# Kernel optimization log

Measured on AMD Instinct MI355X. Metric: run time of the kernel, lower is better.

Reference implementation:

```python
import jax, jax.numpy as jnp
import numpy as np

TOP_K = 2


def setup_inputs() -> dict:
    key = jax.random.key(0)
    k_x, k_g, k_w1, k_w2, k_w3 = jax.random.split(key, 5)
    B, S, D, H, E = 2, 512, 1024, 512, 8
    x = jax.random.normal(k_x, (B, S, D), dtype=jnp.float32)
    gate_w = jax.random.normal(k_g, (D, E), dtype=jnp.float32) * (D ** -0.5)
    w1 = jax.random.normal(k_w1, (E, D, H), dtype=jnp.float32) * 0.02  # gate proj
    w2 = jax.random.normal(k_w2, (E, H, D), dtype=jnp.float32) * 0.02  # down proj
    w3 = jax.random.normal(k_w3, (E, D, H), dtype=jnp.float32) * 0.02  # up proj
    return {"x": x, "gate_w": gate_w, "w1": w1, "w2": w2, "w3": w3}


def reference(x, gate_w, w1, w2, w3):
    # Token-choice top-k MoE with grouped SwiGLU experts, no shared expert.
    # Equivalent to torchtune MoE: gather routed tokens, scale by top-k router
    # score, run per-expert FFN, scatter-add back. Since each expert's FFN has
    # no bias (FFN(0) == 0), the dispatch/grouped-GEMM/combine is expressed
    # densely as sum_e FFN_e(scale[:, e] * x), which is mathematically identical.
    B, S, D = x.shape
    E = gate_w.shape[1]
    xf = x.reshape(B * S, D)                      # [T, D]
    T = B * S

    logits = xf @ gate_w                          # [T, E]
    scores = jax.nn.softmax(logits, axis=-1)
    top_scores, top_idx = jax.lax.top_k(scores, TOP_K)  # [T, k]

    # scale[t, e] = router score if expert e selected for token t, else 0
    scale = jnp.zeros((T, E), dtype=x.dtype).at[
        jnp.arange(T)[:, None], top_idx
    ].set(top_scores)

    xs = scale.T[:, :, None] * xf[None, :, :]     # [E, T, D] scaled routed input
    h = jax.nn.silu(jnp.einsum('etd,edh->eth', xs, w1)) \
        * jnp.einsum('etd,edh->eth', xs, w3)      # [E, T, H]
    y = jnp.einsum('eth,ehd->etd', h, w2)         # [E, T, D]
    out = y.sum(axis=0)                           # combine (scatter-add equiv)
    return out.reshape(B, S, D)
```

## Files before the change

### kernel.cpp

```cpp
#include <hip/hip_runtime.h>
#include <hip/hip_bf16.h>
#include <cstddef>

#define T_TOK 1024
#define D_DIM 1024
#define H_DIM 512
#define E_EXP 8
#define P_CAP 2560
#define MAX_MT (P_CAP / 64)
#define LDA 72

typedef __attribute__((ext_vector_type(4))) float    float4_t;
typedef __attribute__((ext_vector_type(8))) short    short8_t;
typedef __attribute__((ext_vector_type(4))) unsigned uint4_t;

__device__ __forceinline__ short f2bf(float f) {
  union { float f; unsigned u; } v; v.f = f;
  unsigned u = v.u;
  u += 0x7FFFu + ((u >> 16) & 1u);
  return (short)(u >> 16);
}

__device__ __forceinline__ unsigned pkbf(float a, float b) {
  union { __hip_bfloat162 h; unsigned u; } v;
  v.h = __float22bfloat162_rn(make_float2(a, b));
  return v.u;
}

__global__ __launch_bounds__(256) void wconv_kernel(
    const float* __restrict__ w1, const float* __restrict__ w3,
    const float* __restrict__ w2, short* __restrict__ w13t,
    short* __restrict__ w2t) {
  __shared__ float tile[64][68];
  const int z = blockIdx.z;
  const float* src; short* dst; int N, ldd, row_off; size_t ses, des;
  if (z < 16) {
    if (blockIdx.y >= 8) return;
    int which = z >> 3, e = z & 7;
    src = (which ? w3 : w1) + (size_t)e * D_DIM * H_DIM;
    dst = w13t + (size_t)e * D_DIM * (2 * H_DIM);
    N = H_DIM; ldd = D_DIM; row_off = which ? H_DIM : 0;
  } else {
    if (blockIdx.x >= 8) return;
    int e = z - 16;
    src = w2 + (size_t)e * H_DIM * D_DIM;
    dst = w2t + (size_t)e * D_DIM * H_DIM;
    N = D_DIM; ldd = H_DIM; row_off = 0;
  }
  const int k0 = blockIdx.x * 64, n0 = blockIdx.y * 64;
  const int tid = threadIdx.x;
  const int kr = tid >> 4, nc = (tid & 15) * 4;
  #pragma unroll
  for (int p = 0; p < 4; ++p) {
    int k = p * 16 + kr;
    float4_t v = *(const float4_t*)(src + (size_t)(k0 + k) * N + n0 + nc);
    *(float4_t*)&tile[k][nc] = v;
  }
  __syncthreads();
  const int r8 = tid >> 3, c8 = tid & 7;
  #pragma unroll
  for (int p = 0; p < 2; ++p) {
    int row = p * 32 + r8;
    uint4_t u;
    #pragma unroll
    for (int j = 0; j < 4; ++j)
      u[j] = pkbf(tile[c8 * 8 + 2 * j][row], tile[c8 * 8 + 2 * j + 1][row]);
    *(uint4_t*)(dst + (size_t)(row_off + n0 + row) * ldd + k0 + c8 * 8) = u;
  }
}

__global__ __launch_bounds__(256) void router_kernel(
    const float* __restrict__ x, const float* __restrict__ gw,
    int* __restrict__ idx2, float* __restrict__ scale2) {
  const int wid  = threadIdx.x >> 6;
  const int lane = threadIdx.x & 63;
  const int t = blockIdx.x * 4 + wid;
  const float* xr = x + (size_t)t * D_DIM;
  float acc[E_EXP];
  #pragma unroll
  for (int e = 0; e < E_EXP; ++e) acc[e] = 0.f;
  for (int d = lane; d < D_DIM; d += 64) {
    float xv = xr[d];
    float4_t g0 = *(const float4_t*)(gw + d * E_EXP);
    float4_t g1 = *(const float4_t*)(gw + d * E_EXP + 4);
    acc[0] += xv * g0[0]; acc[1] += xv * g0[1];
    acc[2] += xv * g0[2]; acc[3] += xv * g0[3];
    acc[4] += xv * g1[0]; acc[5] += xv * g1[1];
    acc[6] += xv * g1[2]; acc[7] += xv * g1[3];
  }
  #pragma unroll
  for (int off = 32; off >= 1; off >>= 1) {
    #pragma unroll
    for (int e = 0; e < E_EXP; ++e) acc[e] += __shfl_down(acc[e], off, 64);
  }
  if (lane == 0) {
    float m = acc[0];
    #pragma unroll
    for (int e = 1; e < E_EXP; ++e) m = fmaxf(m, acc[e]);
    float p[E_EXP]; float s = 0.f;
    #pragma unroll
    for (int e = 0; e < E_EXP; ++e) { p[e] = __expf(acc[e] - m); s += p[e]; }
    float inv = 1.f / s;
    #pragma unroll
    for (int e = 0; e < E_EXP; ++e) p[e] *= inv;
    int i1 = 0;
    #pragma unroll
    for (int e = 1; e < E_EXP; ++e) if (p[e] > p[i1]) i1 = e;
    int i2 = (i1 == 0) ? 1 : 0;
    #pragma unroll
    for (int e = 0; e < E_EXP; ++e) {
      if (e == i1 || e == i2) continue;
      if (p[e] > p[i2]) i2 = e;
    }
    idx2[2 * t]     = i1;  scale2[2 * t]     = p[i1];
    idx2[2 * t + 1] = i2;  scale2[2 * t + 1] = p[i2];
  }
}

__global__ __launch_bounds__(256) void scan_kernel(
    const int* __restrict__ idx2, const float* __restrict__ scale2,
    int* __restrict__ pair_tok, float* __restrict__ pair_scale,
    int* __restrict__ meta) {
  __shared__ int cnt[E_EXP], base[E_EXP], cur[E_EXP];
  const int tid = threadIdx.x;
  if (tid < E_EXP) { cnt[tid] = 0; cur[tid] = 0; }
  for (int p = tid; p < P_CAP; p += 256) { pair_tok[p] = -1; pair_scale[p] = 0.f; }
  __syncthreads();
  for (int t = tid; t < T_TOK; t += 256) {
    atomicAdd(&cnt[idx2[2 * t]], 1);
    atomicAdd(&cnt[idx2[2 * t + 1]], 1);
  }
  __syncthreads();
  if (tid == 0) {
    int b = 0, g = 0;
    for (int e = 0; e < E_EXP; ++e) {
      base[e] = b;
      int al = (cnt[e] + 63) & ~63;
      for (int j = 0; j < al; j += 64) { meta[1 + g] = e; meta[41 + g] = b + j; ++g; }
      b += al;
    }
    meta[0] = g;
  }
  __syncthreads();
  for (int t = tid; t < T_TOK; t += 256) {
    #pragma unroll
    for (int s = 0; s < 2; ++s) {
      int e = idx2[2 * t + s];
      int p = base[e] + atomicAdd(&cur[e], 1);
      pair_tok[p] = t;
      pair_scale[p] = scale2[2 * t + s];
    }
  }
}

__global__ __launch_bounds__(256) void xsconv_kernel(
    const float* __restrict__ x, const int* __restrict__ pair_tok,
    const float* __restrict__ pair_scale, short* __restrict__ xs) {
  const int row = blockIdx.x * 8 + (threadIdx.x >> 5);
  const int seg = (threadIdx.x & 31) * 32;
  const int tok = pair_tok[row];
  const float sc = pair_scale[row];
  const float* src = x + (size_t)(tok < 0 ? 0 : tok) * D_DIM + seg;
  short* dst = xs + (size_t)row * D_DIM + seg;
  #pragma unroll
  for (int p = 0; p < 2; ++p) {
    float4_t v0 = *(const float4_t*)(src + p * 16);
    float4_t v1 = *(const float4_t*)(src + p * 16 + 4);
    float4_t v2 = *(const float4_t*)(src + p * 16 + 8);
    float4_t v3 = *(const float4_t*)(src + p * 16 + 12);
    uint4_t u0 = {pkbf(v0[0] * sc, v0[1] * sc), pkbf(v0[2] * sc, v0[3] * sc),
                  pkbf(v1[0] * sc, v1[1] * sc), pkbf(v1[2] * sc, v1[3] * sc)};
    uint4_t u1 = {pkbf(v2[0] * sc, v2[1] * sc), pkbf(v2[2] * sc, v2[3] * sc),
                  pkbf(v3[0] * sc, v3[1] * sc), pkbf(v3[2] * sc, v3[3] * sc)};
    *(uint4_t*)(dst + p * 16)     = u0;
    *(uint4_t*)(dst + p * 16 + 8) = u1;
  }
}

__global__ __launch_bounds__(256, 2) void gemm1_kernel(
    const short* __restrict__ xs, const short* __restrict__ w13t,
    const int* __restrict__ meta, short* __restrict__ h) {
  __shared__ short As[2][64 * LDA];
  __shared__ short B1s[2][32 * LDA];
  __shared__ short B3s[2][32 * LDA];
  const int mt = blockIdx.y;
  if (mt >= meta[0]) return;
  const int e    = meta[1 + mt];
  const int row0 = meta[41 + mt];
  const int n0   = blockIdx.x * 32;
  const int tid = threadIdx.x, lane = tid & 63, wid = tid >> 6;
  const int wr = wid >> 1, wc = wid & 1;
  const int q = lane >> 4, ln = lane & 15;
  const short* bsrc = w13t + (size_t)e * D_DIM * (2 * H_DIM);

  const int ar = tid >> 2, ak = (tid & 3) * 16;
  const short* arow = xs + (size_t)(row0 + ar) * D_DIM + ak;
  const int br = tid >> 3, bu = (tid & 7) * 8;
  const short* b1p = bsrc + (size_t)(n0 + br) * D_DIM + bu;
  const short* b3p = bsrc + (size_t)(H_DIM + n0 + br) * D_DIM + bu;

  float4_t acc1[2], acc3[2];
  acc1[0] = acc1[1] = acc3[0] = acc3[1] = (float4_t){0.f, 0.f, 0.f, 0.f};

  uint4_t va0 = *(const uint4_t*)(arow);
  uint4_t va1 = *(const uint4_t*)(arow + 8);
  uint4_t vb1 = *(const uint4_t*)(b1p);
  uint4_t vb3 = *(const uint4_t*)(b3p);
  *(uint4_t*)&As [0][ar * LDA + ak] = va0;
  *(uint4_t*)&As [0][ar * LDA + ak + 8] = va1;
  *(uint4_t*)&B1s[0][br * LDA + bu] = vb1;
  *(uint4_t*)&B3s[0][br * LDA + bu] = vb3;
  __syncthreads();

  for (int k = 0; k < 16; ++k) {
    const int cur = k & 1, nxt = cur ^ 1;
    if (k < 15) {
      int k0 = (k + 1) * 64;
      va0 = *(const uint4_t*)(arow + k0);
      va1 = *(const uint4_t*)(arow + k0 + 8);
      vb1 = *(const uint4_t*)(b1p + k0);
      vb3 = *(const uint4_t*)(b3p + k0);
    }
    short8_t af[2][2], b1f[2], b3f[2];
    #pragma unroll
    for (int i = 0; i < 2; ++i)
      #pragma unroll
      for (int kk = 0; kk < 2; ++kk)
        af[i][kk] = *(const short8_t*)&As[cur][(wr * 32 + i * 16 + ln) * LDA + kk * 32 + q * 8];
    #pragma unroll
    for (int kk = 0; kk < 2; ++kk) {
      b1f[kk] = *(const short8_t*)&B1s[cur][(wc * 16 + ln) * LDA + kk * 32 + q * 8];
      b3f[kk] = *(const short8_t*)&B3s[cur][(wc * 16 + ln) * LDA + kk * 32 + q * 8];
    }
    #pragma unroll
    for (int i = 0; i < 2; ++i)
      #pragma unroll
      for (int kk = 0; kk < 2; ++kk) {
        acc1[i] = __builtin_amdgcn_mfma_f32_16x16x32_bf16(af[i][kk], b1f[kk], acc1[i], 0, 0, 0);
        acc3[i] = __builtin_amdgcn_mfma_f32_16x16x32_bf16(af[i][kk], b3f[kk], acc3[i], 0, 0, 0);
      }
    if (k < 15) {
      *(uint4_t*)&As [nxt][ar * LDA + ak] = va0;
      *(uint4_t*)&As [nxt][ar * LDA + ak + 8] = va1;
      *(uint4_t*)&B1s[nxt][br * LDA + bu] = vb1;
      *(uint4_t*)&B3s[nxt][br * LDA + bu] = vb3;
    }
    __syncthreads();
  }

  #pragma unroll
  for (int i = 0; i < 2; ++i) {
    int r_base = row0 + wr * 32 + i * 16 + q * 4;
    int col = n0 + wc * 16 + ln;
    #pragma unroll
    for (int rr = 0; rr < 4; ++rr) {
      float c1 = acc1[i][rr];
      float c3 = acc3[i][rr];
      float sig = 1.f / (1.f + __expf(-c1));
      h[(size_t)(r_base + rr) * H_DIM + col] = f2bf(c1 * sig * c3);
    }
  }
}

__global__ __launch_bounds__(256, 2) void gemm2_kernel(
    const short* __restrict__ h, const short* __restrict__ w2t,
    const int* __restrict__ pair_tok, const int* __restrict__ meta,
    float* __restrict__ out) {
  __shared__ short As[2][64 * LDA];
  __shared__ short Bs[2][64 * LDA];
  const int mt = blockIdx.y;
  if (mt >= meta[0]) return;
  const int e    = meta[1 + mt];
  const int row0 = meta[41 + mt];
  const int n0   = blockIdx.x * 64;
  const int tid = threadIdx.x, lane = tid & 63, wid = tid >> 6;
  const int wr = wid >> 1, wc = wid & 1;
  const int q = lane >> 4, ln = lane & 15;
  const short* bsrc = w2t + (size_t)e * D_DIM * H_DIM;

  const int ar = tid >> 2, ak = (tid & 3) * 16;
  const short* arow = h + (size_t)(row0 + ar) * H_DIM + ak;
  const short* brow = bsrc + (size_t)(n0 + ar) * H_DIM + ak;

  float4_t acc[2][2];
  #pragma unroll
  for (int i = 0; i < 2; ++i)
    #pragma unroll
    for (int j = 0; j < 2; ++j) acc[i][j] = (float4_t){0.f, 0.f, 0.f, 0.f};

  uint4_t va0 = *(const uint4_t*)(arow);
  uint4_t va1 = *(const uint4_t*)(arow + 8);
  uint4_t vb0 = *(const uint4_t*)(brow);
  uint4_t vb1 = *(const uint4_t*)(brow + 8);
  *(uint4_t*)&As[0][ar * LDA + ak] = va0;
  *(uint4_t*)&As[0][ar * LDA + ak + 8] = va1;
  *(uint4_t*)&Bs[0][ar * LDA + ak] = vb0;
  *(uint4_t*)&Bs[0][ar * LDA + ak + 8] = vb1;
  __syncthreads();

  for (int k = 0; k < 8; ++k) {
    const int cur = k & 1, nxt = cur ^ 1;
    if (k < 7) {
      int k0 = (k + 1) * 64;
      va0 = *(const uint4_t*)(arow + k0);
      va1 = *(const uint4_t*)(arow + k0 + 8);
      vb0 = *(const uint4_t*)(brow + k0);
      vb1 = *(const uint4_t*)(brow + k0 + 8);
    }
    short8_t af[2][2], bf[2][2];
    #pragma unroll
    for (int i = 0; i < 2; ++i)
      #pragma unroll
      for (int kk = 0; kk < 2; ++kk) {
        af[i][kk] = *(const short8_t*)&As[cur][(wr * 32 + i * 16 + ln) * LDA + kk * 32 + q * 8];
        bf[i][kk] = *(const short8_t*)&Bs[cur][(wc * 32 + i * 16 + ln) * LDA + kk * 32 + q * 8];
      }
    #pragma unroll
    for (int i = 0; i < 2; ++i)
      #pragma unroll
      for (int j = 0; j < 2; ++j)
        #pragma unroll
        for (int kk = 0; kk < 2; ++kk)
          acc[i][j] = __builtin_amdgcn_mfma_f32_16x16x32_bf16(af[i][kk], bf[j][kk], acc[i][j], 0, 0, 0);
    if (k < 7) {
      *(uint4_t*)&As[nxt][ar * LDA + ak] = va0;
      *(uint4_t*)&As[nxt][ar * LDA + ak + 8] = va1;
      *(uint4_t*)&Bs[nxt][ar * LDA + ak] = vb0;
      *(uint4_t*)&Bs[nxt][ar * LDA + ak + 8] = vb1;
    }
    __syncthreads();
  }

  #pragma unroll
  for (int i = 0; i < 2; ++i) {
    int r_base = row0 + wr * 32 + i * 16 + q * 4;
    #pragma unroll
    for (int rr = 0; rr < 4; ++rr) {
      int tok = pair_tok[r_base + rr];
      if (tok < 0) continue;
      float* orow = out + (size_t)tok * D_DIM;
      #pragma unroll
      for (int j = 0; j < 2; ++j) {
        int col = n0 + wc * 32 + j * 16 + ln;
        atomicAdd(orow + col, acc[i][j][rr]);
      }
    }
  }
}

extern "C" void kernel_launch(void* const* d_in, const int* in_sizes, int n_in,
                              void* d_out, int out_size, void* d_ws, size_t ws_size,
                              hipStream_t stream) {
  const float* x  = (const float*)d_in[0];
  const float* gw = (const float*)d_in[1];
  const float* w1 = (const float*)d_in[2];
  const float* w2 = (const float*)d_in[3];
  const float* w3 = (const float*)d_in[4];
  float* out = (float*)d_out;

  char* ws = (char*)d_ws;
  int*   idx2    = (int*)  (ws);
  float* scale2  = (float*)(ws + 8192);
  int*   ptok    = (int*)  (ws + 16384);
  float* pscale  = (float*)(ws + 32768);
  int*   meta    = (int*)  (ws + 49152);
  short* xs      = (short*)(ws + (1 << 16));
  short* h       = (short*)(ws + (6u << 20));
  short* w13t    = (short*)(ws + (9u << 20));
  short* w2t     = (short*)(ws + (26u << 20));

  wconv_kernel<<<dim3(16, 16, 24), dim3(256), 0, stream>>>(w1, w3, w2, w13t, w2t);
  router_kernel<<<dim3(T_TOK / 4), dim3(256), 0, stream>>>(x, gw, idx2, scale2);
  scan_kernel<<<dim3(1), dim3(256), 0, stream>>>(idx2, scale2, ptok, pscale, meta);
  xsconv_kernel<<<dim3(P_CAP / 8), dim3(256), 0, stream>>>(x, ptok, pscale, xs);

  gemm1_kernel<<<dim3(H_DIM / 32, MAX_MT), dim3(256), 0, stream>>>(xs, w13t, meta, h);

  hipMemsetAsync(out, 0, (size_t)T_TOK * D_DIM * sizeof(float), stream);
  gemm2_kernel<<<dim3(D_DIM / 64, MAX_MT), dim3(256), 0, stream>>>(h, w2t, ptok, meta, out);
}
```

Before: 152.0 us.

## Merge prep kernels, fuse gather-scale-convert into gemm1, single-buffer GEMM smem

```diff
diff --git a/kernel.cpp b/kernel.cpp
--- a/kernel.cpp
+++ b/kernel.cpp
@@ -27,54 +27,64 @@
   return v.u;
 }
 
-__global__ __launch_bounds__(256) void wconv_kernel(
+__global__ __launch_bounds__(256) void prep_kernel(
     const float* __restrict__ w1, const float* __restrict__ w3,
-    const float* __restrict__ w2, short* __restrict__ w13t,
-    short* __restrict__ w2t) {
+    const float* __restrict__ w2, const float* __restrict__ x,
+    const float* __restrict__ gw, short* __restrict__ w13t,
+    short* __restrict__ w2t, int* __restrict__ idx2,
+    float* __restrict__ scale2, float* __restrict__ out) {
   __shared__ float tile[64][68];
   const int z = blockIdx.z;
-  const float* src; short* dst; int N, ldd, row_off; size_t ses, des;
-  if (z < 16) {
-    if (blockIdx.y >= 8) return;
-    int which = z >> 3, e = z & 7;
-    src = (which ? w3 : w1) + (size_t)e * D_DIM * H_DIM;
-    dst = w13t + (size_t)e * D_DIM * (2 * H_DIM);
-    N = H_DIM; ldd = D_DIM; row_off = which ? H_DIM : 0;
-  } else {
-    if (blockIdx.x >= 8) return;
-    int e = z - 16;
-    src = w2 + (size_t)e * H_DIM * D_DIM;
-    dst = w2t + (size_t)e * D_DIM * H_DIM;
-    N = D_DIM; ldd = H_DIM; row_off = 0;
-  }
-  const int k0 = blockIdx.x * 64, n0 = blockIdx.y * 64;
   const int tid = threadIdx.x;
-  const int kr = tid >> 4, nc = (tid & 15) * 4;
-  #pragma unroll
-  for (int p = 0; p < 4; ++p) {
-    int k = p * 16 + kr;
-    float4_t v = *(const float4_t*)(src + (size_t)(k0 + k) * N + n0 + nc);
-    *(float4_t*)&tile[k][nc] = v;
-  }
-  __syncthreads();
-  const int r8 = tid >> 3, c8 = tid & 7;
-  #pragma unroll
-  for (int p = 0; p < 2; ++p) {
-    int row = p * 32 + r8;
-    uint4_t u;
-    #pragma unroll
-    for (int j = 0; j < 4; ++j)
-      u[j] = pkbf(tile[c8 * 8 + 2 * j][row], tile[c8 * 8 + 2 * j + 1][row]);
-    *(uint4_t*)(dst + (size_t)(row_off + n0 + row) * ldd + k0 + c8 * 8) = u;
-  }
-}
-
-__global__ __launch_bounds__(256) void router_kernel(
-    const float* __restrict__ x, const float* __restrict__ gw,
-    int* __restrict__ idx2, float* __restrict__ scale2) {
-  const int wid  = threadIdx.x >> 6;
-  const int lane = threadIdx.x & 63;
-  const int t = blockIdx.x * 4 + wid;
+
+  if (z < 24) {
+    const float* src; short* dst; int N, ldd, row_off;
+    if (z < 16) {
+      if (blockIdx.y >= 8) return;
+      int which = z >> 3, e = z & 7;
+      src = (which ? w3 : w1) + (size_t)e * D_DIM * H_DIM;
+      dst = w13t + (size_t)e * D_DIM * (2 * H_DIM);
+      N = H_DIM; ldd = D_DIM; row_off = which ? H_DIM : 0;
+    } else {
+      if (blockIdx.x >= 8) return;
+      int e = z - 16;
+      src = w2 + (size_t)e * H_DIM * D_DIM;
+      dst = w2t + (size_t)e * D_DIM * H_DIM;
+      N = D_DIM; ldd = H_DIM; row_off = 0;
+    }
+    const int k0 = blockIdx.x * 64, n0 = blockIdx.y * 64;
+    const int kr = tid >> 4, nc = (tid & 15) * 4;
+    #pragma unroll
+    for (int p = 0; p < 4; ++p) {
+      int k = p * 16 + kr;
+      float4_t v = *(const float4_t*)(src + (size_t)(k0 + k) * N + n0 + nc);
+      *(float4_t*)&tile[k][nc] = v;
+    }
+    __syncthreads();
+    const int r8 = tid >> 3, c8 = tid & 7;
+    #pragma unroll
+    for (int p = 0; p < 2; ++p) {
+      int row = p * 32 + r8;
+      uint4_t u;
+      #pragma unroll
+      for (int j = 0; j < 4; ++j)
+        u[j] = pkbf(tile[c8 * 8 + 2 * j][row], tile[c8 * 8 + 2 * j + 1][row]);
+      *(uint4_t*)(dst + (size_t)(row_off + n0 + row) * ldd + k0 + c8 * 8) = u;
+    }
+    return;
+  }
+
+  if (z == 25) {
+    float4_t z4 = {0.f, 0.f, 0.f, 0.f};
+    float4_t* o = (float4_t*)(out + ((size_t)(blockIdx.y * 16 + blockIdx.x)) * 4096);
+    #pragma unroll
+    for (int i = 0; i < 4; ++i) o[i * 256 + tid] = z4;
+    return;
+  }
+
+  const int wid  = tid >> 6;
+  const int lane = tid & 63;
+  const int t = (blockIdx.y * 16 + blockIdx.x) * 4 + wid;
   const float* xr = x + (size_t)t * D_DIM;
   float acc[E_EXP];
   #pragma unroll
@@ -153,36 +163,13 @@
   }
 }
 
-__global__ __launch_bounds__(256) void xsconv_kernel(
-    const float* __restrict__ x, const int* __restrict__ pair_tok,
-    const float* __restrict__ pair_scale, short* __restrict__ xs) {
-  const int row = blockIdx.x * 8 + (threadIdx.x >> 5);
-  const int seg = (threadIdx.x & 31) * 32;
-  const int tok = pair_tok[row];
-  const float sc = pair_scale[row];
-  const float* src = x + (size_t)(tok < 0 ? 0 : tok) * D_DIM + seg;
-  short* dst = xs + (size_t)row * D_DIM + seg;
-  #pragma unroll
-  for (int p = 0; p < 2; ++p) {
-    float4_t v0 = *(const float4_t*)(src + p * 16);
-    float4_t v1 = *(const float4_t*)(src + p * 16 + 4);
-    float4_t v2 = *(const float4_t*)(src + p * 16 + 8);
-    float4_t v3 = *(const float4_t*)(src + p * 16 + 12);
-    uint4_t u0 = {pkbf(v0[0] * sc, v0[1] * sc), pkbf(v0[2] * sc, v0[3] * sc),
-                  pkbf(v1[0] * sc, v1[1] * sc), pkbf(v1[2] * sc, v1[3] * sc)};
-    uint4_t u1 = {pkbf(v2[0] * sc, v2[1] * sc), pkbf(v2[2] * sc, v2[3] * sc),
-                  pkbf(v3[0] * sc, v3[1] * sc), pkbf(v3[2] * sc, v3[3] * sc)};
-    *(uint4_t*)(dst + p * 16)     = u0;
-    *(uint4_t*)(dst + p * 16 + 8) = u1;
-  }
-}
-
-__global__ __launch_bounds__(256, 2) void gemm1_kernel(
-    const short* __restrict__ xs, const short* __restrict__ w13t,
+__global__ __launch_bounds__(256, 4) void gemm1_kernel(
+    const float* __restrict__ x, const short* __restrict__ w13t,
+    const int* __restrict__ pair_tok, const float* __restrict__ pair_scale,
     const int* __restrict__ meta, short* __restrict__ h) {
-  __shared__ short As[2][64 * LDA];
-  __shared__ short B1s[2][32 * LDA];
-  __shared__ short B3s[2][32 * LDA];
+  __shared__ short As[64 * LDA];
+  __shared__ short B1s[32 * LDA];
+  __shared__ short B3s[32 * LDA];
   const int mt = blockIdx.y;
   if (mt >= meta[0]) return;
   const int e    = meta[1 + mt];
@@ -194,7 +181,9 @@
   const short* bsrc = w13t + (size_t)e * D_DIM * (2 * H_DIM);
 
   const int ar = tid >> 2, ak = (tid & 3) * 16;
-  const short* arow = xs + (size_t)(row0 + ar) * D_DIM + ak;
+  const int   tokr = pair_tok[row0 + ar];
+  const float sc   = pair_scale[row0 + ar];
+  const float* xrow = x + (size_t)(tokr < 0 ? 0 : tokr) * D_DIM + ak;
   const int br = tid >> 3, bu = (tid & 7) * 8;
   const short* b1p = bsrc + (size_t)(n0 + br) * D_DIM + bu;
   const short* b3p = bsrc + (size_t)(H_DIM + n0 + br) * D_DIM + bu;
@@ -202,35 +191,33 @@
   float4_t acc1[2], acc3[2];
   acc1[0] = acc1[1] = acc3[0] = acc3[1] = (float4_t){0.f, 0.f, 0.f, 0.f};
 
-  uint4_t va0 = *(const uint4_t*)(arow);
-  uint4_t va1 = *(const uint4_t*)(arow + 8);
-  uint4_t vb1 = *(const uint4_t*)(b1p);
-  uint4_t vb3 = *(const uint4_t*)(b3p);
-  *(uint4_t*)&As [0][ar * LDA + ak] = va0;
-  *(uint4_t*)&As [0][ar * LDA + ak + 8] = va1;
-  *(uint4_t*)&B1s[0][br * LDA + bu] = vb1;
-  *(uint4_t*)&B3s[0][br * LDA + bu] = vb3;
-  __syncthreads();
-
-  for (int k = 0; k < 16; ++k) {
-    const int cur = k & 1, nxt = cur ^ 1;
-    if (k < 15) {
-      int k0 = (k + 1) * 64;
-      va0 = *(const uint4_t*)(arow + k0);
-      va1 = *(const uint4_t*)(arow + k0 + 8);
-      vb1 = *(const uint4_t*)(b1p + k0);
-      vb3 = *(const uint4_t*)(b3p + k0);
-    }
+  for (int k0 = 0; k0 < D_DIM; k0 += 64) {
+    float4_t v0 = *(const float4_t*)(xrow + k0);
+    float4_t v1 = *(const float4_t*)(xrow + k0 + 4);
+    float4_t v2 = *(const float4_t*)(xrow + k0 + 8);
+    float4_t v3 = *(const float4_t*)(xrow + k0 + 12);
+    uint4_t vb1 = *(const uint4_t*)(b1p + k0);
+    uint4_t vb3 = *(const uint4_t*)(b3p + k0);
+    uint4_t u0 = {pkbf(v0[0] * sc, v0[1] * sc), pkbf(v0[2] * sc, v0[3] * sc),
+                  pkbf(v1[0] * sc, v1[1] * sc), pkbf(v1[2] * sc, v1[3] * sc)};
+    uint4_t u1 = {pkbf(v2[0] * sc, v2[1] * sc), pkbf(v2[2] * sc, v2[3] * sc),
+                  pkbf(v3[0] * sc, v3[1] * sc), pkbf(v3[2] * sc, v3[3] * sc)};
+    *(uint4_t*)&As[ar * LDA + ak]     = u0;
+    *(uint4_t*)&As[ar * LDA + ak + 8] = u1;
+    *(uint4_t*)&B1s[br * LDA + bu] = vb1;
+    *(uint4_t*)&B3s[br * LDA + bu] = vb3;
+    __syncthreads();
+
     short8_t af[2][2], b1f[2], b3f[2];
     #pragma unroll
     for (int i = 0; i < 2; ++i)
       #pragma unroll
       for (int kk = 0; kk < 2; ++kk)
-        af[i][kk] = *(const short8_t*)&As[cur][(wr * 32 + i * 16 + ln) * LDA + kk * 32 + q * 8];
+        af[i][kk] = *(const short8_t*)&As[(wr * 32 + i * 16 + ln) * LDA + kk * 32 + q * 8];
     #pragma unroll
     for (int kk = 0; kk < 2; ++kk) {
-      b1f[kk] = *(const short8_t*)&B1s[cur][(wc * 16 + ln) * LDA + kk * 32 + q * 8];
-      b3f[kk] = *(const short8_t*)&B3s[cur][(wc * 16 + ln) * LDA + kk * 32 + q * 8];
+      b1f[kk] = *(const short8_t*)&B1s[(wc * 16 + ln) * LDA + kk * 32 + q * 8];
+      b3f[kk] = *(const short8_t*)&B3s[(wc * 16 + ln) * LDA + kk * 32 + q * 8];
     }
     #pragma unroll
     for (int i = 0; i < 2; ++i)
@@ -239,12 +226,6 @@
         acc1[i] = __builtin_amdgcn_mfma_f32_16x16x32_bf16(af[i][kk], b1f[kk], acc1[i], 0, 0, 0);
         acc3[i] = __builtin_amdgcn_mfma_f32_16x16x32_bf16(af[i][kk], b3f[kk], acc3[i], 0, 0, 0);
       }
-    if (k < 15) {
-      *(uint4_t*)&As [nxt][ar * LDA + ak] = va0;
-      *(uint4_t*)&As [nxt][ar * LDA + ak + 8] = va1;
-      *(uint4_t*)&B1s[nxt][br * LDA + bu] = vb1;
-      *(uint4_t*)&B3s[nxt][br * LDA + bu] = vb3;
-    }
     __syncthreads();
   }
 
@@ -262,12 +243,12 @@
   }
 }
 
-__global__ __launch_bounds__(256, 2) void gemm2_kernel(
+__global__ __launch_bounds__(256, 4) void gemm2_kernel(
     const short* __restrict__ h, const short* __restrict__ w2t,
     const int* __restrict__ pair_tok, const int* __restrict__ meta,
     float* __restrict__ out) {
-  __shared__ short As[2][64 * LDA];
-  __shared__ short Bs[2][64 * LDA];
+  __shared__ short As[64 * LDA];
+  __shared__ short Bs[64 * LDA];
   const int mt = blockIdx.y;
   if (mt >= meta[0]) return;
   const int e    = meta[1 + mt];
@@ -288,32 +269,24 @@
     #pragma unroll
     for (int j = 0; j < 2; ++j) acc[i][j] = (float4_t){0.f, 0.f, 0.f, 0.f};
 
-  uint4_t va0 = *(const uint4_t*)(arow);
-  uint4_t va1 = *(const uint4_t*)(arow + 8);
-  uint4_t vb0 = *(const uint4_t*)(brow);
-  uint4_t vb1 = *(const uint4_t*)(brow + 8);
-  *(uint4_t*)&As[0][ar * LDA + ak] = va0;
-  *(uint4_t*)&As[0][ar * LDA + ak + 8] = va1;
-  *(uint4_t*)&Bs[0][ar * LDA + ak] = vb0;
-  *(uint4_t*)&Bs[0][ar * LDA + ak + 8] = vb1;
-  __syncthreads();
-
-  for (int k = 0; k < 8; ++k) {
-    const int cur = k & 1, nxt = cur ^ 1;
-    if (k < 7) {
-      int k0 = (k + 1) * 64;
-      va0 = *(const uint4_t*)(arow + k0);
-      va1 = *(const uint4_t*)(arow + k0 + 8);
-      vb0 = *(const uint4_t*)(brow + k0);
-      vb1 = *(const uint4_t*)(brow + k0 + 8);
-    }
+  for (int k0 = 0; k0 < H_DIM; k0 += 64) {
+    uint4_t va0 = *(const uint4_t*)(arow + k0);
+    uint4_t va1 = *(const uint4_t*)(arow + k0 + 8);
+    uint4_t vb0 = *(const uint4_t*)(brow + k0);
+    uint4_t vb1 = *(const uint4_t*)(brow + k0 + 8);
+    *(uint4_t*)&As[ar * LDA + ak]     = va0;
+    *(uint4_t*)&As[ar * LDA + ak + 8] = va1;
+    *(uint4_t*)&Bs[ar * LDA + ak]     = vb0;
+    *(uint4_t*)&Bs[ar * LDA + ak + 8] = vb1;
+    __syncthreads();
+
     short8_t af[2][2], bf[2][2];
     #pragma unroll
     for (int i = 0; i < 2; ++i)
       #pragma unroll
       for (int kk = 0; kk < 2; ++kk) {
-        af[i][kk] = *(const short8_t*)&As[cur][(wr * 32 + i * 16 + ln) * LDA + kk * 32 + q * 8];
-        bf[i][kk] = *(const short8_t*)&Bs[cur][(wc * 32 + i * 16 + ln) * LDA + kk * 32 + q * 8];
+        af[i][kk] = *(const short8_t*)&As[(wr * 32 + i * 16 + ln) * LDA + kk * 32 + q * 8];
+        bf[i][kk] = *(const short8_t*)&Bs[(wc * 32 + i * 16 + ln) * LDA + kk * 32 + q * 8];
       }
     #pragma unroll
     for (int i = 0; i < 2; ++i)
@@ -322,12 +295,6 @@
         #pragma unroll
         for (int kk = 0; kk < 2; ++kk)
           acc[i][j] = __builtin_amdgcn_mfma_f32_16x16x32_bf16(af[i][kk], bf[j][kk], acc[i][j], 0, 0, 0);
-    if (k < 7) {
-      *(uint4_t*)&As[nxt][ar * LDA + ak] = va0;
-      *(uint4_t*)&As[nxt][ar * LDA + ak + 8] = va1;
-      *(uint4_t*)&Bs[nxt][ar * LDA + ak] = vb0;
-      *(uint4_t*)&Bs[nxt][ar * LDA + ak + 8] = vb1;
-    }
     __syncthreads();
   }
 
@@ -364,18 +331,15 @@
   int*   ptok    = (int*)  (ws + 16384);
   float* pscale  = (float*)(ws + 32768);
   int*   meta    = (int*)  (ws + 49152);
-  short* xs      = (short*)(ws + (1 << 16));
-  short* h       = (short*)(ws + (6u << 20));
-  short* w13t    = (short*)(ws + (9u << 20));
-  short* w2t     = (short*)(ws + (26u << 20));
-
-  wconv_kernel<<<dim3(16, 16, 24), dim3(256), 0, stream>>>(w1, w3, w2, w13t, w2t);
-  router_kernel<<<dim3(T_TOK / 4), dim3(256), 0, stream>>>(x, gw, idx2, scale2);
+  short* h       = (short*)(ws + (1u << 20));
+  short* w13t    = (short*)(ws + (4u << 20));
+  short* w2t     = (short*)(ws + (21u << 20));
+
+  prep_kernel<<<dim3(16, 16, 26), dim3(256), 0, stream>>>(
+      w1, w3, w2, x, gw, w13t, w2t, idx2, scale2, out);
   scan_kernel<<<dim3(1), dim3(256), 0, stream>>>(idx2, scale2, ptok, pscale, meta);
-  xsconv_kernel<<<dim3(P_CAP / 8), dim3(256), 0, stream>>>(x, ptok, pscale, xs);
-
-  gemm1_kernel<<<dim3(H_DIM / 32, MAX_MT), dim3(256), 0, stream>>>(xs, w13t, meta, h);
-
-  hipMemsetAsync(out, 0, (size_t)T_TOK * D_DIM * sizeof(float), stream);
-  gemm2_kernel<<<dim3(D_DIM / 64, MAX_MT), dim3(256), 0, stream>>>(h, w2t, ptok, meta, out);
-}
+  gemm1_kernel<<<dim3(H_DIM / 32, MAX_MT), dim3(256), 0, stream>>>(
+      x, w13t, ptok, pscale, meta, h);
+  gemm2_kernel<<<dim3(D_DIM / 64, MAX_MT), dim3(256), 0, stream>>>(
+      h, w2t, ptok, meta, out);
+}
```

New measurement: 150.7 us. No clear change (-0.8%).
